# Optimization experiments

Measured on AMD Instinct MI355X. Metric: run time of the kernel, lower is better.

The kernel has to match this reference:

```python
import jax, jax.numpy as jnp
import numpy as np

HEIGHT = 1024.0
WIDTH = 1024.0
OUTER_BOUND_WEIGHT = 0.01


def setup_inputs() -> dict:
    key = jax.random.key(0)
    k1, k2 = jax.random.split(key)
    B, K = 4096, 4096
    # predictions roughly in-image scale
    output = jax.random.normal(k1, (B, K, 2), dtype=jnp.float32) * 300.0 + 512.0
    target = jax.random.uniform(k2, (B, K, 2), dtype=jnp.float32) * 1224.0 - 100.0
    return {"output": output, "target": target}


def reference(output, target):
    # output, target: [B, K, 2]
    B = target.shape[0]
    tx = target[..., 0]
    ty = target[..., 1]
    oob = (tx < 0) | (tx > WIDTH) | (ty < 0) | (ty > HEIGHT)  # [B, K]
    weight = jnp.where(oob, OUTER_BOUND_WEIGHT, 1.0).astype(output.dtype)
    sq = jnp.sum((output - target) ** 2, axis=-1)  # [B, K] per-keypoint MSE
    raw_batch_loss = jnp.sum(weight * sq)
    return raw_batch_loss / B
```

## Files before the change

kernel.cpp:

```cpp
#include <hip/hip_runtime.h>


#define WIDTH_F  1024.0f
#define HEIGHT_F 1024.0f
#define OOB_W    0.01f
#define NB 16
#define U_RES 13

typedef float f32x4 __attribute__((ext_vector_type(4)));

__device__ __forceinline__ float kp_pair(f32x4 o, f32x4 t) {
    float dx = o[0] - t[0];
    float dy = o[1] - t[1];
    float sqA = dx * dx + dy * dy;
    bool oobA = (t[0] < 0.0f) || (t[0] > WIDTH_F) || (t[1] < 0.0f) || (t[1] > HEIGHT_F);
    float dz = o[2] - t[2];
    float dw = o[3] - t[3];
    float sqB = dz * dz + dw * dw;
    bool oobB = (t[2] < 0.0f) || (t[2] > WIDTH_F) || (t[3] < 0.0f) || (t[3] > HEIGHT_F);
    return (oobA ? OOB_W : 1.0f) * sqA + (oobB ? OOB_W : 1.0f) * sqB;
}

__global__ __launch_bounds__(256) void res_kp_loss_kernel(
    const f32x4* __restrict__ out4,
    const f32x4* __restrict__ tgt4,
    float* __restrict__ result,
    int n4,
    float inv_b) {
    const int idx    = blockIdx.x * blockDim.x + threadIdx.x;
    const int stride = gridDim.x * blockDim.x;

    float acc[4];
    acc[0] = acc[1] = acc[2] = acc[3] = 0.0f;

    int i = idx;
    if (idx + (NB - 1) * stride < n4) {
        f32x4 t[NB], o[NB];
        #pragma unroll
        for (int u = 0; u < NB; ++u) {
            const f32x4* p = &tgt4[idx + u * stride];
            t[u] = (u < U_RES) ? *p : __builtin_nontemporal_load(p);
        }
        #pragma unroll
        for (int u = 0; u < NB; ++u) o[u] = out4[idx + u * stride];
        asm volatile("" ::: "memory");
        #pragma unroll
        for (int u = 0; u < NB; ++u) acc[u & 3] += kp_pair(o[u], t[u]);
        i = idx + NB * stride;
    }
    for (; i < n4; i += stride)
        acc[0] += kp_pair(out4[i], tgt4[i]);

    float accs = (acc[0] + acc[1]) + (acc[2] + acc[3]);

    #pragma unroll
    for (int off = 32; off > 0; off >>= 1)
        accs += __shfl_down(accs, off, 64);

    __shared__ float wave_sums[4];
    int lane = threadIdx.x & 63;
    int wave = threadIdx.x >> 6;
    if (lane == 0) wave_sums[wave] = accs;
    __syncthreads();

    if (threadIdx.x == 0) {
        float s = (wave_sums[0] + wave_sums[1]) + (wave_sums[2] + wave_sums[3]);
        atomicAdd(result, s * inv_b);
    }
}

extern "C" void kernel_launch(void* const* d_in, const int* in_sizes, int n_in,
                              void* d_out, int out_size, void* d_ws, size_t ws_size,
                              hipStream_t stream) {
    const f32x4* out4 = (const f32x4*)d_in[0];
    const f32x4* tgt4 = (const f32x4*)d_in[1];
    float* result = (float*)d_out;

    const int total_floats = in_sizes[0];
    const int n4 = total_floats / 4;
    const float inv_b = 1.0f / 4096.0f;

    hipMemsetAsync(d_out, 0, out_size * sizeof(float), stream);

    const int block = 256;
    const int grid = 2048;
    res_kp_loss_kernel<<<grid, block, 0, stream>>>(out4, tgt4, result, n4, inv_b);
}
```

Baseline: 283.4 us.

## Software-pipeline loads with inline-asm nontemporal dwordx4 and explicit vmcnt waits

Replaces the load-all-then-compute block with a staged pipeline. Each stage issues four nontemporal global_load_dwordx4 through inline asm, then waits with s_waitcnt vmcnt(4) so the previous stage can be consumed while the next stage's loads are in flight. It also makes every load nontemporal, dropping the earlier split where part of the target loads were cached, and the tail loop now uses nontemporal loads as well. The risk is that hand-placed waitcnt and sched_barrier limit memory-level parallelism compared with issuing all 32 loads up front. It also bypasses compiler scheduling, and the compiler's own waitcnt insertion may interact with the asm loads.

```diff
diff --git a/kernel.cpp b/kernel.cpp
--- a/kernel.cpp
+++ b/kernel.cpp
@@ -5,9 +5,14 @@
 #define HEIGHT_F 1024.0f
 #define OOB_W    0.01f
 #define NB 16
-#define U_RES 13
+#define NSTEP 8
+#define PAIRS 2
 
 typedef float f32x4 __attribute__((ext_vector_type(4)));
+
+#define LOADX4_NT(dst, base, voff)                                   \
+    asm volatile("global_load_dwordx4 %0, %1, %2 nt"                 \
+                 : "=&v"(dst) : "v"(voff), "s"(base))
 
 __device__ __forceinline__ float kp_pair(f32x4 o, f32x4 t) {
     float dx = o[0] - t[0];
@@ -36,20 +41,59 @@
     int i = idx;
     if (idx + (NB - 1) * stride < n4) {
         f32x4 t[NB], o[NB];
+
+        #define ISSUE(s)                                                      \
+            do {                                                              \
+                unsigned v0 = (unsigned)(idx + (2 * (s)) * stride) * 16u;     \
+                unsigned v1 = (unsigned)(idx + (2 * (s) + 1) * stride) * 16u; \
+                LOADX4_NT(t[2 * (s)],     tgt4, v0);                          \
+                LOADX4_NT(t[2 * (s) + 1], tgt4, v1);                          \
+                LOADX4_NT(o[2 * (s)],     out4, v0);                          \
+                LOADX4_NT(o[2 * (s) + 1], out4, v1);                          \
+            } while (0)
+
+        #define CONSUME(s)                                                    \
+            do {                                                              \
+                acc[(2 * (s)) & 3]     += kp_pair(o[2 * (s)],     t[2 * (s)]);\
+                acc[(2 * (s) + 1) & 3] += kp_pair(o[2 * (s) + 1], t[2 * (s) + 1]); \
+            } while (0)
+
+        ISSUE(0);
         #pragma unroll
-        for (int u = 0; u < NB; ++u) {
-            const f32x4* p = &tgt4[idx + u * stride];
-            t[u] = (u < U_RES) ? *p : __builtin_nontemporal_load(p);
+        for (int s = 0; s < NSTEP; ++s) {
+            if (s + 1 < NSTEP) {
+                switch (s + 1) {
+                    case 1: ISSUE(1); break;
+                    case 2: ISSUE(2); break;
+                    case 3: ISSUE(3); break;
+                    case 4: ISSUE(4); break;
+                    case 5: ISSUE(5); break;
+                    case 6: ISSUE(6); break;
+                    case 7: ISSUE(7); break;
+                }
+                asm volatile("s_waitcnt vmcnt(4)" ::: "memory");
+            } else {
+                asm volatile("s_waitcnt vmcnt(0)" ::: "memory");
+            }
+            __builtin_amdgcn_sched_barrier(0);
+            switch (s) {
+                case 0: CONSUME(0); break;
+                case 1: CONSUME(1); break;
+                case 2: CONSUME(2); break;
+                case 3: CONSUME(3); break;
+                case 4: CONSUME(4); break;
+                case 5: CONSUME(5); break;
+                case 6: CONSUME(6); break;
+                case 7: CONSUME(7); break;
+            }
         }
-        #pragma unroll
-        for (int u = 0; u < NB; ++u) o[u] = out4[idx + u * stride];
-        asm volatile("" ::: "memory");
-        #pragma unroll
-        for (int u = 0; u < NB; ++u) acc[u & 3] += kp_pair(o[u], t[u]);
+        #undef ISSUE
+        #undef CONSUME
         i = idx + NB * stride;
     }
     for (; i < n4; i += stride)
-        acc[0] += kp_pair(out4[i], tgt4[i]);
+        acc[0] += kp_pair(__builtin_nontemporal_load(&out4[i]),
+                          __builtin_nontemporal_load(&tgt4[i]));
 
     float accs = (acc[0] + acc[1]) + (acc[2] + acc[3]);
 
```

Result: faster. 257.4 us (-9.2%).
